# Kernel tuning notes

Measured on AMD Instinct MI355X. Metric: run time of the kernel, lower is better.

Reference implementation:

```python
import jax, jax.numpy as jnp
import numpy as np

AGENT_RADIUS = 0.2
SAFETY_DIST = 0.1
_ang = np.linspace(0.0, 2.0 * np.pi, 8, endpoint=False)
OBSTACLES = np.stack([10.0 * np.cos(_ang), 10.0 * np.sin(_ang), 0.5 * np.ones(8)], axis=-1).astype(np.float32)  # (x, y, r)


def _qp_solve(p, G, h):
    """Exact solve of: min_z 0.5 z^T z + p^T z  s.t. G z <= h, z in R^2.
    Equivalent to QPFunction with Q=I. Enumerates KKT candidates over active
    sets of size 0, 1, 2 (closed form in 2D) and picks the feasible optimum.
    p: [2], G: [m,2], h: [m]."""
    m = G.shape[0]
    ii, jj = np.triu_indices(m, 1)
    # active set {} -> unconstrained minimizer
    z0 = -p[None, :]                                        # [1,2]
    # active set {i}: z = -p - lam*g_i, g_i.z = h_i
    gg = jnp.sum(G * G, axis=-1)                            # [m]
    lam1 = (-(G @ p) - h) / (gg + 1e-12)
    z1 = -p[None, :] - lam1[:, None] * G                    # [m,2]
    ok1 = lam1 >= -1e-8
    # active set {i,j}: z solves 2x2 system [g_i; g_j] z = [h_i; h_j]
    Gi, Gj = G[ii], G[jj]                                   # [P,2]
    hi, hj = h[ii], h[jj]
    det = Gi[:, 0] * Gj[:, 1] - Gi[:, 1] * Gj[:, 0]
    det_ok = jnp.abs(det) > 1e-9
    ds = jnp.where(det_ok, det, 1.0)
    zx = (hi * Gj[:, 1] - hj * Gi[:, 1]) / ds
    zy = (Gi[:, 0] * hj - Gj[:, 0] * hi) / ds
    z2 = jnp.stack([zx, zy], axis=-1)                       # [P,2]
    r = -(z2 + p[None, :])                                  # A^T lam = r
    lam_i = (Gj[:, 1] * r[:, 0] - Gj[:, 0] * r[:, 1]) / ds
    lam_j = (Gi[:, 0] * r[:, 1] - Gi[:, 1] * r[:, 0]) / ds
    ok2 = det_ok & (lam_i >= -1e-8) & (lam_j >= -1e-8)
    Z = jnp.concatenate([z0, z1, z2], axis=0)               # [K,2]
    ok = jnp.concatenate([jnp.ones((1,), bool), ok1, ok2], axis=0)
    tol = 1e-6 * (1.0 + jnp.abs(h))
    feas = jnp.all(Z @ G.T <= (h + tol)[None, :], axis=-1)  # [K]
    obj = 0.5 * jnp.sum(Z * Z, axis=-1) + Z @ p
    obj = jnp.where(ok & feas, obj, jnp.inf)
    return Z[jnp.argmin(obj)]


def _forward(x, mean, std, W1, b1, W21, b21, W31, b31, W22, b22, W32, b32):
    x0 = x * std + mean                                     # de-normalized state [B,8]
    hid = jax.nn.relu(x @ W1.T + b1)
    x31 = jax.nn.relu(hid @ W21.T + b21) @ W31.T + b31      # reference control p [B,2]
    x32 = 4.0 * jax.nn.sigmoid(jax.nn.relu(hid @ W22.T + b22) @ W32.T + b32)  # CBF penalties [B,2]
    px, py, theta, v = x0[:, 0], x0[:, 1], x0[:, 2], x0[:, 3]
    ox, oy, oth, ov = x0[:, 4], x0[:, 5], x0[:, 6], x0[:, 7]
    st, ct = jnp.sin(theta), jnp.cos(theta)
    vs, vc = v * st, v * ct
    obs = jnp.asarray(OBSTACLES, x.dtype)
    # static obstacle constraints, vectorized over the n_obs obstacles
    dx = px[:, None] - obs[None, :, 0]                      # [B,n_obs]
    dy = py[:, None] - obs[None, :, 1]
    R = AGENT_RADIUS + obs[:, 2] + SAFETY_DIST
    bar = dx * dx + dy * dy - (R * R)[None, :]
    bdot = 2.0 * dx * vc[:, None] + 2.0 * dy * vs[:, None]
    Lf2b = (2.0 * v * v)[:, None]
    u1 = -2.0 * dx * vs[:, None] + 2.0 * dy * vc[:, None]
    u2 = 2.0 * dx * ct[:, None] + 2.0 * dy * st[:, None]
    G_obs = -jnp.stack([u1, u2], axis=-1)                   # [B,n_obs,2]
    s0, s1 = x32[:, 0:1], x32[:, 1:2]
    h_obs = Lf2b + (s0 + s1) * bdot + (s0 * s1) * bar       # [B,n_obs]
    # opponent constraint
    Ro = 2.0 * AGENT_RADIUS + SAFETY_DIST
    dxo, dyo = px - ox, py - oy
    so, co = jnp.sin(oth), jnp.cos(oth)
    bar_o = dxo * dxo + dyo * dyo - Ro * Ro
    bdot_o = 2.0 * dxo * (vc - ov * co) + 2.0 * dyo * (vs - ov * so)
    Lf2b_o = 2.0 * (v * v + ov * ov + 2.0 * v * ov * jnp.cos(theta - oth))
    u1o = -2.0 * dxo * vs + 2.0 * dyo * vc
    u2o = 2.0 * dxo * ct + 2.0 * dyo * st
    G_opp = -jnp.stack([u1o, u2o], axis=-1)[:, None, :]     # [B,1,2]
    h_opp = (Lf2b_o + (x32[:, 0] + x32[:, 1]) * bdot_o + x32[:, 0] * x32[:, 1] * bar_o)[:, None]
    G = jnp.concatenate([G_obs, G_opp], axis=1)             # [B,m,2]
    h = jnp.concatenate([h_obs, h_opp], axis=1)             # [B,m]
    return jax.vmap(_qp_solve)(x31, G, h)                   # [B,2]


def setup_inputs() -> dict:
    key = jax.random.key(0)
    ks = jax.random.split(key, 6)
    B, nF, H1, H2 = 65536, 8, 256, 128

    def lin(k, o, i):
        k1, k2 = jax.random.split(k)
        W = jax.random.normal(k1, (o, i), jnp.float32) / np.float32(np.sqrt(i))
        b = jax.random.normal(k2, (o,), jnp.float32) * 0.01
        return W, b

    W1, b1 = lin(ks[0], H1, nF)
    W21, b21 = lin(ks[1], H2, H1)
    W31, b31 = lin(ks[2], 2, H2)
    W22, b22 = lin(ks[3], H2, H1)
    W32, b32 = lin(ks[4], 2, H2)
    x = jax.random.normal(ks[5], (B, nF), jnp.float32)
    return {"x": x, "mean": jnp.zeros((nF,), jnp.float32), "std": jnp.ones((nF,), jnp.float32),
            "W1": W1, "b1": b1, "W21": W21, "b21": b21, "W31": W31, "b31": b31,
            "W22": W22, "b22": b22, "W32": W32, "b32": b32, "sgn": 1}


def reference(x, mean, std, W1, b1, W21, b21, W31, b31, W22, b22, W32, b32, sgn):
    # sgn==1 / training path -> batched differentiable QP solve
    return _forward(x, mean, std, W1, b1, W21, b21, W31, b31, W22, b22, W32, b32)
```

## Files before the change

### kernel.cpp

```cpp
#include <hip/hip_runtime.h>
#include <hip/hip_bf16.h>
#include <math.h>


typedef unsigned int u32;
typedef unsigned long long u64;
typedef unsigned short u16;
typedef __attribute__((ext_vector_type(8))) short short8;
typedef __attribute__((ext_vector_type(4))) float f32x4;
typedef __attribute__((ext_vector_type(2))) float f32x2;
typedef __attribute__((ext_vector_type(4))) u32 u32x4;

union Frag  { short8 v; u32 u[4]; u32x4 q; };
union F8    { long l; u32 u[2]; };

__device__ __forceinline__ u32 packbf(float a, float b) {
    float2 f2; f2.x = a; f2.y = b;
    __hip_bfloat162 h = __float22bfloat162_rn(f2);
    union { __hip_bfloat162 h2; u32 u; } cv; cv.h2 = h;
    return cv.u;
}

__device__ __forceinline__ u32 packfp8x4(float a, float b, float c, float d) {
    u32 r = 0;
    r = (u32)__builtin_amdgcn_cvt_pk_fp8_f32(a, b, (int)r, false);
    r = (u32)__builtin_amdgcn_cvt_pk_fp8_f32(c, d, (int)r, true);
    return r;
}

__device__ const float OBX[8] = { 10.f, 7.07106781186547524f, 6.123234e-16f, -7.07106781186547524f,
                                 -10.f, -7.07106781186547524f, -1.8369702e-15f, 7.07106781186547524f };
__device__ const float OBY[8] = { 0.f, 7.07106781186547524f, 10.f, 7.07106781186547524f,
                                  1.2246468e-15f, -7.07106781186547524f, -10.f, -7.07106781186547524f };

#define PI0_ 0x2111111100000000ULL
#define PI1_ 0x5544443333322222ULL
#define PI2_ 0x7665ULL
#define PJ0_ 0x3876543287654321ULL
#define PJ1_ 0x7687658765487654ULL
#define PJ2_ 0x8878ULL
__device__ __forceinline__ int unpack4(u64 w0, u64 w1, u64 w2, int t) {
    u64 w = (t < 16) ? w0 : (t < 32) ? w1 : w2;
    return (int)((w >> ((t & 15) * 4)) & 15);
}

__global__ __launch_bounds__(256)
void prep_kernel(const float* __restrict__ W21, const float* __restrict__ W22,
                 const float* __restrict__ W1,  const float* __restrict__ b1,
                 u32* __restrict__ ws)
{
    int idx  = blockIdx.x * 256 + threadIdx.x;
    if (idx < 4096) {
        int lane = idx & 63;
        int nt   = (idx >> 6) & 7;
        int kp   = (idx >> 9) & 3;
        int head = idx >> 11;
        const float* W = head ? W22 : W21;
        int q  = lane >> 4;
        int n  = nt * 16 + (lane & 15);
        const float* se = W + n * 256 + (2 * kp) * 32 + q * 8;
        const float* so = W + n * 256 + (2 * kp + 1) * 32 + q * 8;
        u32x4 o;
        o.x = packfp8x4(se[0], se[1], se[2], se[3]);
        o.y = packfp8x4(se[4], se[5], se[6], se[7]);
        o.z = packfp8x4(so[0], so[1], so[2], so[3]);
        o.w = packfp8x4(so[4], so[5], so[6], so[7]);
        __builtin_nontemporal_store(o, (u32x4*)ws + idx);
    } else {
        int f    = idx - 4096;
        int nt   = f >> 6;
        int lane = f & 63;
        int q    = lane >> 4;
        int mm   = lane & 15;
        int n = 32 * (nt & 7) + 8 * (mm >> 2) + 4 * (nt >> 3) + (mm & 3);
        u32x4 o = (u32x4){0u, 0u, 0u, 0u};
        if (q == 0) {
            const float* wr = W1 + n * 8;
            o.x = packbf(wr[0], wr[1]);
            o.y = packbf(wr[2], wr[3]);
            o.z = packbf(wr[4], wr[5]);
            o.w = packbf(wr[6], wr[7]);
        } else if (q == 1) {
            o.x = packbf(b1[n], 0.f);
        }
        __builtin_nontemporal_store(o, (u32x4*)ws + idx);
    }
}

__global__ __launch_bounds__(512)
void barriernet_kernel(const float* __restrict__ x,
                       const float* __restrict__ meanp,
                       const float* __restrict__ stdp,
                       const float* __restrict__ b21,
                       const float* __restrict__ W31,
                       const float* __restrict__ b31,
                       const float* __restrict__ b22,
                       const float* __restrict__ W32,
                       const float* __restrict__ b32,
                       const u32* __restrict__ wsB,
                       float* __restrict__ out, int Btot)
{
    const int tid  = threadIdx.x;
    const int wave = tid >> 6;
    const int lane = tid & 63;
    const int q    = lane >> 4;
    const int m    = lane & 15;
    const int blockRow = blockIdx.x * 128;

    __shared__ u32x4 stage[4096];
    __shared__ float lds_p[128][4];

    const u32x4* wsB4 = (const u32x4*)wsB;

    #pragma unroll
    for (int i = 0; i < 8; ++i) {
        int fi = (wave * 8 + i) * 64 + lane;
        stage[fi] = wsB4[fi];
    }

    Frag xB;
    {
        int R0 = blockRow + wave * 16 + m;
        const f32x4* xv0 = (const f32x4*)(x + (R0 < Btot ? R0 : 0) * 8);
        f32x4 xa0 = xv0[0], xb0 = xv0[1];
        if (q == 0) {
            xB.u[0] = packbf(xa0.x, xa0.y);
            xB.u[1] = packbf(xa0.z, xa0.w);
            xB.u[2] = packbf(xb0.x, xb0.y);
            xB.u[3] = packbf(xb0.z, xb0.w);
        } else if (q == 1) {
            xB.u[0] = 0x00003f80u;
            xB.u[1] = 0u; xB.u[2] = 0u; xB.u[3] = 0u;
        } else {
            xB.u[0] = 0u; xB.u[1] = 0u; xB.u[2] = 0u; xB.u[3] = 0u;
        }
    }
    f32x4 hacc[16];
    {
        const u32x4* W1f = wsB4 + 4096;
        #pragma unroll
        for (int nt = 0; nt < 16; ++nt) {
            Frag Af; Af.q = W1f[nt * 64 + lane];
            hacc[nt] = __builtin_amdgcn_mfma_f32_16x16x32_bf16(
                Af.v, xB.v, (f32x4){0.f, 0.f, 0.f, 0.f}, 0, 0, 0);
        }
    }
    F8 A8[8];
    #pragma unroll
    for (int ks = 0; ks < 8; ++ks) {
        A8[ks].u[0] = packfp8x4(fmaxf(hacc[ks][0], 0.f),     fmaxf(hacc[ks][1], 0.f),
                                fmaxf(hacc[ks][2], 0.f),     fmaxf(hacc[ks][3], 0.f));
        A8[ks].u[1] = packfp8x4(fmaxf(hacc[ks + 8][0], 0.f), fmaxf(hacc[ks + 8][1], 0.f),
                                fmaxf(hacc[ks + 8][2], 0.f), fmaxf(hacc[ks + 8][3], 0.f));
    }

    __syncthreads();

    #pragma unroll 1
    for (int head = 0; head < 2; ++head) {
        const float* b2 = head ? b22 : b21;
        const float* W3 = head ? W32 : W31;
        const float* b3 = head ? b32 : b31;

        f32x4 acc[8];
        #pragma unroll
        for (int nt = 0; nt < 8; ++nt) acc[nt] = (f32x4){0.f, 0.f, 0.f, 0.f};

        const u32x4* hS = stage + head * 2048;
        #pragma unroll
        for (int kp = 0; kp < 4; ++kp) {
            #pragma unroll
            for (int nt = 0; nt < 8; ++nt) {
                u32x4 b = hS[kp * 512 + nt * 64 + lane];
                F8 be; be.u[0] = b.x; be.u[1] = b.y;
                F8 bo; bo.u[0] = b.z; bo.u[1] = b.w;
                acc[nt] = __builtin_amdgcn_mfma_f32_16x16x32_fp8_fp8(
                    A8[2 * kp].l, be.l, acc[nt], 0, 0, 0);
                acc[nt] = __builtin_amdgcn_mfma_f32_16x16x32_fp8_fp8(
                    A8[2 * kp + 1].l, bo.l, acc[nt], 0, 0, 0);
            }
        }

        float pr0[4], pr1[4];
        #pragma unroll
        for (int rg = 0; rg < 4; ++rg) { pr0[rg] = 0.f; pr1[rg] = 0.f; }
        #pragma unroll
        for (int nt = 0; nt < 8; ++nt) {
            int col = nt * 16 + m;
            float b2c = b2[col];
            float w0c = W3[col];
            float w1c = W3[128 + col];
            #pragma unroll
            for (int rg = 0; rg < 4; ++rg) {
                float rv = fmaxf(acc[nt][rg] + b2c, 0.f);
                pr0[rg] = fmaf(rv, w0c, pr0[rg]);
                pr1[rg] = fmaf(rv, w1c, pr1[rg]);
            }
        }
        #pragma unroll
        for (int rg = 0; rg < 4; ++rg) {
            float v0 = pr0[rg], v1 = pr1[rg];
            #pragma unroll
            for (int off = 1; off < 16; off <<= 1) {
                v0 += __shfl_xor(v0, off, 64);
                v1 += __shfl_xor(v1, off, 64);
            }
            pr0[rg] = v0; pr1[rg] = v1;
        }
        if (m == 0) {
            #pragma unroll
            for (int rg = 0; rg < 4; ++rg) {
                int row = wave * 16 + q * 4 + rg;
                float a0 = pr0[rg] + b3[0];
                float a1 = pr1[rg] + b3[1];
                if (head == 0) {
                    lds_p[row][0] = a0;
                    lds_p[row][1] = a1;
                } else {
                    lds_p[row][2] = 4.f / (1.f + __expf(-a0));
                    lds_p[row][3] = 4.f / (1.f + __expf(-a1));
                }
            }
        }
    }
    __syncthreads();

    f32x4 (*qC)[128]  = (f32x4(*)[128])stage;
    f32x4 (*res)[128] = (f32x4(*)[128])(stage + 1152);

    const int rq   = tid & 127;
    const int part = tid >> 7;
    const int R    = blockRow + rq;
    float p0 = lds_p[rq][0];
    float p1 = lds_p[rq][1];

    {
        float s0 = lds_p[rq][2];
        float s1 = lds_p[rq][3];
        const float* xp = x + (R < Btot ? R : 0) * 8;
        f32x4 xv0 = ((const f32x4*)xp)[0];
        f32x4 xv1 = ((const f32x4*)xp)[1];
        const f32x4 sd0 = ((const f32x4*)stdp)[0],  sd1 = ((const f32x4*)stdp)[1];
        const f32x4 mn0 = ((const f32x4*)meanp)[0], mn1 = ((const f32x4*)meanp)[1];
        float px = fmaf(xv0.x, sd0.x, mn0.x);
        float py = fmaf(xv0.y, sd0.y, mn0.y);
        float th = fmaf(xv0.z, sd0.z, mn0.z);
        float v  = fmaf(xv0.w, sd0.w, mn0.w);
        float st = __sinf(th), ct = __cosf(th);
        float vs = v * st, vc = v * ct;
        float sps = s0 + s1, ss = s0 * s1;
        float Lf2b = 2.f * v * v;
        #pragma unroll
        for (int kk = 0; kk < 2; ++kk) {
            int k = part + kk * 4;
            float dx = px - OBX[k], dy = py - OBY[k];
            float bar  = dx * dx + dy * dy - 0.64f;
            float bdot = 2.f * dx * vc + 2.f * dy * vs;
            float gx = 2.f * dx * vs - 2.f * dy * vc;
            float gy = -(2.f * dx * ct + 2.f * dy * st);
            float hk = Lf2b + sps * bdot + ss * bar;
            float ht = hk + 1e-6f * (1.f + fabsf(hk));
            qC[k][rq] = (f32x4){gx, gy, hk, ht};
        }
        if (part == 3) {
            float ox = fmaf(xv1.x, sd1.x, mn1.x);
            float oy = fmaf(xv1.y, sd1.y, mn1.y);
            float oth= fmaf(xv1.z, sd1.z, mn1.z);
            float ov = fmaf(xv1.w, sd1.w, mn1.w);
            float so = __sinf(oth), co = __cosf(oth);
            float dxo = px - ox, dyo = py - oy;
            float bar_o  = dxo * dxo + dyo * dyo - 0.25f;
            float bdot_o = 2.f * dxo * (vc - ov * co) + 2.f * dyo * (vs - ov * so);
            float Lf2b_o = 2.f * (v * v + ov * ov + 2.f * v * ov * __cosf(th - oth));
            float gx = 2.f * dxo * vs - 2.f * dyo * vc;
            float gy = -(2.f * dxo * ct + 2.f * dyo * st);
            float hk = Lf2b_o + sps * bdot_o + ss * bar_o;
            float ht = hk + 1e-6f * (1.f + fabsf(hk));
            qC[8][rq] = (f32x4){gx, gy, hk, ht};
        }
    }
    __syncthreads();

    const f32x4 C0 = qC[0][rq], C1 = qC[1][rq], C2 = qC[2][rq];
    const f32x4 C3 = qC[3][rq], C4 = qC[4][rq], C5 = qC[5][rq];
    const f32x4 C6 = qC[6][rq], C7 = qC[7][rq], C8 = qC[8][rq];

    const float zx0 = -p0, zy0 = -p1;
    bool z0ok =
        (zx0 * C0.x + zy0 * C0.y <= C0.w) &&
        (zx0 * C1.x + zy0 * C1.y <= C1.w) &&
        (zx0 * C2.x + zy0 * C2.y <= C2.w) &&
        (zx0 * C3.x + zy0 * C3.y <= C3.w) &&
        (zx0 * C4.x + zy0 * C4.y <= C4.w) &&
        (zx0 * C5.x + zy0 * C5.y <= C5.w) &&
        (zx0 * C6.x + zy0 * C6.y <= C6.w) &&
        (zx0 * C7.x + zy0 * C7.y <= C7.w) &&
        (zx0 * C8.x + zy0 * C8.y <= C8.w);

    float bobj = INFINITY;
    float bzx = zx0, bzy = zy0;
    if (z0ok) {
        if (part == 0)
            bobj = 0.5f * (zx0 * zx0 + zy0 * zy0) + zx0 * p0 + zy0 * p1;
    } else {
        const int c0i = (part == 0) ? 0  : (part == 1) ? 12 : (part == 2) ? 24 : 35;
        const int c1i = (part == 0) ? 12 : (part == 1) ? 24 : (part == 2) ? 35 : 46;
        #pragma unroll 2
        for (int c = c0i; c < c1i; ++c) {
            float zx, zy;
            bool pre;
            if (c == 0) {
                zx = -p0; zy = -p1; pre = true;
            } else if (c <= 9) {
                f32x4 g = qC[c - 1][rq];
                float gg  = g.x * g.x + g.y * g.y;
                float lam = (-(g.x * p0 + g.y * p1) - g.z) / (gg + 1e-12f);
                zx = -p0 - lam * g.x;
                zy = -p1 - lam * g.y;
                pre = (lam >= -1e-8f);
            } else {
                int t = c - 10;
                int pi = unpack4(PI0_, PI1_, PI2_, t);
                int pj = unpack4(PJ0_, PJ1_, PJ2_, t);
                f32x4 gi = qC[pi][rq];
                f32x4 gj = qC[pj][rq];
                float det = gi.x * gj.y - gi.y * gj.x;
                bool dok = fabsf(det) > 1e-9f;
                float ds = dok ? det : 1.0f;
                float inv = 1.0f / ds;
                zx = (gi.z * gj.y - gj.z * gi.y) * inv;
                zy = (gi.x * gj.z - gj.x * gi.z) * inv;
                float rx = -(zx + p0), ry = -(zy + p1);
                float li = (gj.y * rx - gj.x * ry) * inv;
                float lj = (gi.x * ry - gi.y * rx) * inv;
                pre = dok && (li >= -1e-8f) && (lj >= -1e-8f);
            }
            bool ok = pre;
            ok = ok && (zx * C0.x + zy * C0.y <= C0.w);
            ok = ok && (zx * C1.x + zy * C1.y <= C1.w);
            ok = ok && (zx * C2.x + zy * C2.y <= C2.w);
            ok = ok && (zx * C3.x + zy * C3.y <= C3.w);
            ok = ok && (zx * C4.x + zy * C4.y <= C4.w);
            ok = ok && (zx * C5.x + zy * C5.y <= C5.w);
            ok = ok && (zx * C6.x + zy * C6.y <= C6.w);
            ok = ok && (zx * C7.x + zy * C7.y <= C7.w);
            ok = ok && (zx * C8.x + zy * C8.y <= C8.w);
            float obj = 0.5f * (zx * zx + zy * zy) + zx * p0 + zy * p1;
            if (ok && obj < bobj) { bobj = obj; bzx = zx; bzy = zy; }
        }
    }

    if (part) {
        res[part - 1][rq] = (f32x4){bobj, bzx, bzy, 0.f};
    }
    __syncthreads();
    if (part == 0) {
        #pragma unroll
        for (int pp = 0; pp < 3; ++pp) {
            f32x4 r = res[pp][rq];
            if (r.x < bobj) { bobj = r.x; bzx = r.y; bzy = r.z; }
        }
        if (R < Btot) {
            f32x2 o2; o2.x = bzx; o2.y = bzy;
            ((f32x2*)out)[R] = o2;
        }
    }
}

extern "C" void kernel_launch(void* const* d_in, const int* in_sizes, int n_in,
                              void* d_out, int out_size, void* d_ws, size_t ws_size,
                              hipStream_t stream) {
    const float* x    = (const float*)d_in[0];
    const float* mean = (const float*)d_in[1];
    const float* stdv = (const float*)d_in[2];
    const float* W1   = (const float*)d_in[3];
    const float* b1   = (const float*)d_in[4];
    const float* W21  = (const float*)d_in[5];
    const float* b21  = (const float*)d_in[6];
    const float* W31  = (const float*)d_in[7];
    const float* b31  = (const float*)d_in[8];
    const float* W22  = (const float*)d_in[9];
    const float* b22  = (const float*)d_in[10];
    const float* W32  = (const float*)d_in[11];
    const float* b32  = (const float*)d_in[12];
    int B = in_sizes[0] / 8;
    float* out = (float*)d_out;
    u32* ws = (u32*)d_ws;

    hipLaunchKernelGGL(prep_kernel, dim3(20), dim3(256), 0, stream,
                       W21, W22, W1, b1, ws);

    hipLaunchKernelGGL(barriernet_kernel, dim3((B + 127) / 128), dim3(512), 0, stream,
                       x, mean, stdv, b21, W31, b31, b22, W32, b32,
                       ws, out, B);
}
```

Measured before the change: 103.8 us.

## Switch MLP to 32x32 MFMA tiles with 256-thread blocks and DMA weight staging

Recasts the fused MLP to use 32x32xK MFMA instructions, so each wave handles 32 rows and blocks shrink from 512 to 256 threads. Prep reorders the fp8 W2 fragments, the bf16 W1 fragments and the layer-3 weights and biases into matching 32x32 layouts. The final 2-output projection now runs as a bf16 MFMA instead of scalar FMAs plus cross-lane shuffles. Weights are staged into LDS with global_load_lds DMA. The QP enumeration is split over 2 parts instead of 4, so each thread does more candidates and there are fewer threads per row.

```diff
diff --git a/kernel.cpp b/kernel.cpp
--- a/kernel.cpp
+++ b/kernel.cpp
@@ -8,11 +8,23 @@
 typedef unsigned short u16;
 typedef __attribute__((ext_vector_type(8))) short short8;
 typedef __attribute__((ext_vector_type(4))) float f32x4;
+typedef __attribute__((ext_vector_type(16))) float f32x16;
 typedef __attribute__((ext_vector_type(2))) float f32x2;
 typedef __attribute__((ext_vector_type(4))) u32 u32x4;
 
 union Frag  { short8 v; u32 u[4]; u32x4 q; };
 union F8    { long l; u32 u[2]; };
+
+__device__ __forceinline__ f32x16 zero16() {
+    f32x16 z = {0.f, 0.f, 0.f, 0.f, 0.f, 0.f, 0.f, 0.f,
+                0.f, 0.f, 0.f, 0.f, 0.f, 0.f, 0.f, 0.f};
+    return z;
+}
+
+#define DMA16(gp, lp)                                                        \
+    __builtin_amdgcn_global_load_lds(                                        \
+        (const __attribute__((address_space(1))) void*)(gp),                 \
+        (__attribute__((address_space(3))) void*)(lp), 16, 0, 0)
 
 __device__ __forceinline__ u32 packbf(float a, float b) {
     float2 f2; f2.x = a; f2.y = b;
@@ -20,7 +32,6 @@
     union { __hip_bfloat162 h2; u32 u; } cv; cv.h2 = h;
     return cv.u;
 }
-
 __device__ __forceinline__ u32 packfp8x4(float a, float b, float c, float d) {
     u32 r = 0;
     r = (u32)__builtin_amdgcn_cvt_pk_fp8_f32(a, b, (int)r, false);
@@ -47,55 +58,77 @@
 __global__ __launch_bounds__(256)
 void prep_kernel(const float* __restrict__ W21, const float* __restrict__ W22,
                  const float* __restrict__ W1,  const float* __restrict__ b1,
+                 const float* __restrict__ W31, const float* __restrict__ W32,
+                 const float* __restrict__ b21, const float* __restrict__ b22,
                  u32* __restrict__ ws)
 {
-    int idx  = blockIdx.x * 256 + threadIdx.x;
+    int idx = blockIdx.x * 256 + threadIdx.x;
     if (idx < 4096) {
         int lane = idx & 63;
-        int nt   = (idx >> 6) & 7;
-        int kp   = (idx >> 9) & 3;
+        int nt   = (idx >> 6) & 3;
+        int kp   = (idx >> 8) & 7;
         int head = idx >> 11;
         const float* W = head ? W22 : W21;
-        int q  = lane >> 4;
-        int n  = nt * 16 + (lane & 15);
-        const float* se = W + n * 256 + (2 * kp) * 32 + q * 8;
-        const float* so = W + n * 256 + (2 * kp + 1) * 32 + q * 8;
-        u32x4 o;
-        o.x = packfp8x4(se[0], se[1], se[2], se[3]);
-        o.y = packfp8x4(se[4], se[5], se[6], se[7]);
-        o.z = packfp8x4(so[0], so[1], so[2], so[3]);
-        o.w = packfp8x4(so[4], so[5], so[6], so[7]);
-        __builtin_nontemporal_store(o, (u32x4*)ws + idx);
-    } else {
-        int f    = idx - 4096;
-        int nt   = f >> 6;
+        int o  = nt * 32 + (lane & 31);
+        int hi = lane >> 5;
+        const float* base = W + o * 256 + kp * 32 + hi * 4;
+        u32x4 e;
+        e.x = packfp8x4(base[0],  base[1],  base[2],  base[3]);
+        e.y = packfp8x4(base[8],  base[9],  base[10], base[11]);
+        e.z = packfp8x4(base[16], base[17], base[18], base[19]);
+        e.w = packfp8x4(base[24], base[25], base[26], base[27]);
+        __builtin_nontemporal_store(e, (u32x4*)ws + idx);
+    } else if (idx < 4608) {
+        int f = idx - 4096;
+        int inst = f >> 6, lane = f & 63;
+        int hi = lane >> 5;
+        int h  = inst * 32 + (lane & 31);
+        u32x4 e = (u32x4){0u, 0u, 0u, 0u};
+        if (hi == 0) {
+            const float* wr = W1 + h * 8;
+            e.x = packbf(wr[0], wr[1]);
+            e.y = packbf(wr[2], wr[3]);
+            e.z = packbf(wr[4], wr[5]);
+            e.w = packbf(wr[6], wr[7]);
+        } else {
+            e.x = packbf(b1[h], 0.f);
+        }
+        __builtin_nontemporal_store(e, (u32x4*)ws + idx);
+    } else if (idx < 5632) {
+        int f = idx - 4608;
+        int head = f >> 9;
+        int kb   = (f >> 6) & 7;
         int lane = f & 63;
-        int q    = lane >> 4;
-        int mm   = lane & 15;
-        int n = 32 * (nt & 7) + 8 * (mm >> 2) + 4 * (nt >> 3) + (mm & 3);
-        u32x4 o = (u32x4){0u, 0u, 0u, 0u};
-        if (q == 0) {
-            const float* wr = W1 + n * 8;
-            o.x = packbf(wr[0], wr[1]);
-            o.y = packbf(wr[2], wr[3]);
-            o.z = packbf(wr[4], wr[5]);
-            o.w = packbf(wr[6], wr[7]);
-        } else if (q == 1) {
-            o.x = packbf(b1[n], 0.f);
-        }
-        __builtin_nontemporal_store(o, (u32x4*)ws + idx);
-    }
-}
-
-__global__ __launch_bounds__(512)
+        int hi = lane >> 5;
+        int mr = lane & 31;
+        const float* W3 = head ? W32 : W31;
+        int ob = 32 * (kb >> 1) + 16 * (kb & 1) + 4 * hi;
+        float v0=0, v1=0, v2=0, v3=0, v4=0, v5=0, v6=0, v7=0;
+        if (mr < 2) {
+            const float* wr = W3 + mr * 128;
+            v0 = wr[ob];     v1 = wr[ob + 1]; v2 = wr[ob + 2]; v3 = wr[ob + 3];
+            v4 = wr[ob + 8]; v5 = wr[ob + 9]; v6 = wr[ob + 10]; v7 = wr[ob + 11];
+        }
+        u32x4 e;
+        e.x = packbf(v0, v1); e.y = packbf(v2, v3);
+        e.z = packbf(v4, v5); e.w = packbf(v6, v7);
+        __builtin_nontemporal_store(e, (u32x4*)ws + idx);
+    } else if (idx < 5696) {
+        int f = idx - 5632;
+        int head = f >> 5, hi = (f >> 4) & 1, nt = (f >> 2) & 3, t = f & 3;
+        const float* b2 = head ? b22 : b21;
+        int o0 = nt * 32 + 8 * t + 4 * hi;
+        f32x4 e; e.x = b2[o0]; e.y = b2[o0+1]; e.z = b2[o0+2]; e.w = b2[o0+3];
+        union { f32x4 f; u32x4 u; } cv; cv.f = e;
+        __builtin_nontemporal_store(cv.u, (u32x4*)ws + idx);
+    }
+}
+
+__global__ __launch_bounds__(256)
 void barriernet_kernel(const float* __restrict__ x,
                        const float* __restrict__ meanp,
                        const float* __restrict__ stdp,
-                       const float* __restrict__ b21,
-                       const float* __restrict__ W31,
                        const float* __restrict__ b31,
-                       const float* __restrict__ b22,
-                       const float* __restrict__ W32,
                        const float* __restrict__ b32,
                        const u32* __restrict__ wsB,
                        float* __restrict__ out, int Btot)
@@ -103,8 +136,8 @@
     const int tid  = threadIdx.x;
     const int wave = tid >> 6;
     const int lane = tid & 63;
-    const int q    = lane >> 4;
-    const int m    = lane & 15;
+    const int hi   = lane >> 5;
+    const int ml   = lane & 31;
     const int blockRow = blockIdx.x * 128;
 
     __shared__ u32x4 stage[4096];
@@ -112,114 +145,125 @@
 
     const u32x4* wsB4 = (const u32x4*)wsB;
 
-    #pragma unroll
-    for (int i = 0; i < 8; ++i) {
-        int fi = (wave * 8 + i) * 64 + lane;
-        stage[fi] = wsB4[fi];
+    {
+        const u32x4* g0 = wsB4 + wave * 1024 + lane;
+        u32x4* l0 = stage + wave * 1024;
+        #pragma unroll
+        for (int i = 0; i < 16; ++i)
+            DMA16(g0 + i * 64, l0 + i * 64);
     }
 
     Frag xB;
     {
-        int R0 = blockRow + wave * 16 + m;
+        int R0 = blockRow + wave * 32 + ml;
         const f32x4* xv0 = (const f32x4*)(x + (R0 < Btot ? R0 : 0) * 8);
         f32x4 xa0 = xv0[0], xb0 = xv0[1];
-        if (q == 0) {
+        if (hi == 0) {
             xB.u[0] = packbf(xa0.x, xa0.y);
             xB.u[1] = packbf(xa0.z, xa0.w);
             xB.u[2] = packbf(xb0.x, xb0.y);
             xB.u[3] = packbf(xb0.z, xb0.w);
-        } else if (q == 1) {
+        } else {
             xB.u[0] = 0x00003f80u;
             xB.u[1] = 0u; xB.u[2] = 0u; xB.u[3] = 0u;
-        } else {
-            xB.u[0] = 0u; xB.u[1] = 0u; xB.u[2] = 0u; xB.u[3] = 0u;
-        }
-    }
-    f32x4 hacc[16];
-    {
-        const u32x4* W1f = wsB4 + 4096;
-        #pragma unroll
-        for (int nt = 0; nt < 16; ++nt) {
-            Frag Af; Af.q = W1f[nt * 64 + lane];
-            hacc[nt] = __builtin_amdgcn_mfma_f32_16x16x32_bf16(
-                Af.v, xB.v, (f32x4){0.f, 0.f, 0.f, 0.f}, 0, 0, 0);
-        }
-    }
-    F8 A8[8];
+        }
+    }
+    F8 B8[16];
     #pragma unroll
-    for (int ks = 0; ks < 8; ++ks) {
-        A8[ks].u[0] = packfp8x4(fmaxf(hacc[ks][0], 0.f),     fmaxf(hacc[ks][1], 0.f),
-                                fmaxf(hacc[ks][2], 0.f),     fmaxf(hacc[ks][3], 0.f));
-        A8[ks].u[1] = packfp8x4(fmaxf(hacc[ks + 8][0], 0.f), fmaxf(hacc[ks + 8][1], 0.f),
-                                fmaxf(hacc[ks + 8][2], 0.f), fmaxf(hacc[ks + 8][3], 0.f));
+    for (int chunk = 0; chunk < 2; ++chunk) {
+        f32x16 hacc[4];
+        #pragma unroll
+        for (int i2 = 0; i2 < 4; ++i2) {
+            int inst = chunk * 4 + i2;
+            Frag W1f; W1f.q = wsB4[4096 + inst * 64 + lane];
+            hacc[i2] = __builtin_amdgcn_mfma_f32_32x32x16_bf16(
+                W1f.v, xB.v, zero16(), 0, 0, 0);
+        }
+        #pragma unroll
+        for (int k2 = 0; k2 < 8; ++k2) {
+            int ks = chunk * 8 + k2;
+            int i2 = k2 >> 1;
+            int pb = 8 * (k2 & 1);
+            B8[ks].u[0] = packfp8x4(fmaxf(hacc[i2][pb+0], 0.f), fmaxf(hacc[i2][pb+1], 0.f),
+                                    fmaxf(hacc[i2][pb+2], 0.f), fmaxf(hacc[i2][pb+3], 0.f));
+            B8[ks].u[1] = packfp8x4(fmaxf(hacc[i2][pb+4], 0.f), fmaxf(hacc[i2][pb+5], 0.f),
+                                    fmaxf(hacc[i2][pb+6], 0.f), fmaxf(hacc[i2][pb+7], 0.f));
+        }
     }
 
     __syncthreads();
 
     #pragma unroll 1
     for (int head = 0; head < 2; ++head) {
-        const float* b2 = head ? b22 : b21;
-        const float* W3 = head ? W32 : W31;
-        const float* b3 = head ? b32 : b31;
-
-        f32x4 acc[8];
-        #pragma unroll
-        for (int nt = 0; nt < 8; ++nt) acc[nt] = (f32x4){0.f, 0.f, 0.f, 0.f};
+        f32x16 acc[4];
+        #pragma unroll
+        for (int nt = 0; nt < 4; ++nt) acc[nt] = zero16();
 
         const u32x4* hS = stage + head * 2048;
         #pragma unroll
-        for (int kp = 0; kp < 4; ++kp) {
+        for (int kp = 0; kp < 8; ++kp) {
             #pragma unroll
-            for (int nt = 0; nt < 8; ++nt) {
-                u32x4 b = hS[kp * 512 + nt * 64 + lane];
-                F8 be; be.u[0] = b.x; be.u[1] = b.y;
-                F8 bo; bo.u[0] = b.z; bo.u[1] = b.w;
-                acc[nt] = __builtin_amdgcn_mfma_f32_16x16x32_fp8_fp8(
-                    A8[2 * kp].l, be.l, acc[nt], 0, 0, 0);
-                acc[nt] = __builtin_amdgcn_mfma_f32_16x16x32_fp8_fp8(
-                    A8[2 * kp + 1].l, bo.l, acc[nt], 0, 0, 0);
+            for (int nt = 0; nt < 4; ++nt) {
+                u32x4 e = hS[kp * 256 + nt * 64 + lane];
+                F8 ae; ae.u[0] = e.x; ae.u[1] = e.y;
+                F8 ao; ao.u[0] = e.z; ao.u[1] = e.w;
+                acc[nt] = __builtin_amdgcn_mfma_f32_32x32x16_fp8_fp8(
+                    ae.l, B8[2 * kp].l, acc[nt], 0, 0, 0);
+                acc[nt] = __builtin_amdgcn_mfma_f32_32x32x16_fp8_fp8(
+                    ao.l, B8[2 * kp + 1].l, acc[nt], 0, 0, 0);
             }
         }
 
-        float pr0[4], pr1[4];
-        #pragma unroll
-        for (int rg = 0; rg < 4; ++rg) { pr0[rg] = 0.f; pr1[rg] = 0.f; }
-        #pragma unroll
-        for (int nt = 0; nt < 8; ++nt) {
-            int col = nt * 16 + m;
-            float b2c = b2[col];
-            float w0c = W3[col];
-            float w1c = W3[128 + col];
-            #pragma unroll
-            for (int rg = 0; rg < 4; ++rg) {
-                float rv = fmaxf(acc[nt][rg] + b2c, 0.f);
-                pr0[rg] = fmaf(rv, w0c, pr0[rg]);
-                pr1[rg] = fmaf(rv, w1c, pr1[rg]);
-            }
-        }
-        #pragma unroll
-        for (int rg = 0; rg < 4; ++rg) {
-            float v0 = pr0[rg], v1 = pr1[rg];
-            #pragma unroll
-            for (int off = 1; off < 16; off <<= 1) {
-                v0 += __shfl_xor(v0, off, 64);
-                v1 += __shfl_xor(v1, off, 64);
-            }
-            pr0[rg] = v0; pr1[rg] = v1;
-        }
-        if (m == 0) {
-            #pragma unroll
-            for (int rg = 0; rg < 4; ++rg) {
-                int row = wave * 16 + q * 4 + rg;
-                float a0 = pr0[rg] + b3[0];
-                float a1 = pr1[rg] + b3[1];
-                if (head == 0) {
-                    lds_p[row][0] = a0;
-                    lds_p[row][1] = a1;
-                } else {
-                    lds_p[row][2] = 4.f / (1.f + __expf(-a0));
-                    lds_p[row][3] = 4.f / (1.f + __expf(-a1));
-                }
+        const f32x4* b2p = (const f32x4*)(wsB4 + 5632 + head * 32 + hi * 16);
+        Frag rvB[8];
+        #pragma unroll
+        for (int nt = 0; nt < 4; ++nt) {
+            f32x4 bq0 = b2p[nt * 4 + 0];
+            f32x4 bq1 = b2p[nt * 4 + 1];
+            f32x4 bq2 = b2p[nt * 4 + 2];
+            f32x4 bq3 = b2p[nt * 4 + 3];
+            float rv0  = fmaxf(acc[nt][0]  + bq0.x, 0.f);
+            float rv1  = fmaxf(acc[nt][1]  + bq0.y, 0.f);
+            float rv2  = fmaxf(acc[nt][2]  + bq0.z, 0.f);
+            float rv3  = fmaxf(acc[nt][3]  + bq0.w, 0.f);
+            float rv4  = fmaxf(acc[nt][4]  + bq1.x, 0.f);
+            float rv5  = fmaxf(acc[nt][5]  + bq1.y, 0.f);
+            float rv6  = fmaxf(acc[nt][6]  + bq1.z, 0.f);
+            float rv7  = fmaxf(acc[nt][7]  + bq1.w, 0.f);
+            float rv8  = fmaxf(acc[nt][8]  + bq2.x, 0.f);
+            float rv9  = fmaxf(acc[nt][9]  + bq2.y, 0.f);
+            float rv10 = fmaxf(acc[nt][10] + bq2.z, 0.f);
+            float rv11 = fmaxf(acc[nt][11] + bq2.w, 0.f);
+            float rv12 = fmaxf(acc[nt][12] + bq3.x, 0.f);
+            float rv13 = fmaxf(acc[nt][13] + bq3.y, 0.f);
+            float rv14 = fmaxf(acc[nt][14] + bq3.z, 0.f);
+            float rv15 = fmaxf(acc[nt][15] + bq3.w, 0.f);
+            rvB[nt * 2 + 0].u[0] = packbf(rv0,  rv1);
+            rvB[nt * 2 + 0].u[1] = packbf(rv2,  rv3);
+            rvB[nt * 2 + 0].u[2] = packbf(rv4,  rv5);
+            rvB[nt * 2 + 0].u[3] = packbf(rv6,  rv7);
+            rvB[nt * 2 + 1].u[0] = packbf(rv8,  rv9);
+            rvB[nt * 2 + 1].u[1] = packbf(rv10, rv11);
+            rvB[nt * 2 + 1].u[2] = packbf(rv12, rv13);
+            rvB[nt * 2 + 1].u[3] = packbf(rv14, rv15);
+        }
+        f32x16 acc3 = zero16();
+        #pragma unroll
+        for (int kb = 0; kb < 8; ++kb) {
+            Frag W3f; W3f.q = wsB4[4608 + head * 512 + kb * 64 + lane];
+            acc3 = __builtin_amdgcn_mfma_f32_32x32x16_bf16(
+                W3f.v, rvB[kb].v, acc3, 0, 0, 0);
+        }
+        if (hi == 0) {
+            int row = wave * 32 + ml;
+            if (head == 0) {
+                lds_p[row][0] = acc3[0] + b31[0];
+                lds_p[row][1] = acc3[1] + b31[1];
+            } else {
+                float a0 = acc3[0] + b32[0];
+                float a1 = acc3[1] + b32[1];
+                lds_p[row][2] = 4.f / (1.f + __expf(-a0));
+                lds_p[row][3] = 4.f / (1.f + __expf(-a1));
             }
         }
     }
@@ -251,8 +295,8 @@
         float sps = s0 + s1, ss = s0 * s1;
         float Lf2b = 2.f * v * v;
         #pragma unroll
-        for (int kk = 0; kk < 2; ++kk) {
-            int k = part + kk * 4;
+        for (int kk = 0; kk < 4; ++kk) {
+            int k = part * 4 + kk;
             float dx = px - OBX[k], dy = py - OBY[k];
             float bar  = dx * dx + dy * dy - 0.64f;
             float bdot = 2.f * dx * vc + 2.f * dy * vs;
@@ -262,7 +306,7 @@
             float ht = hk + 1e-6f * (1.f + fabsf(hk));
             qC[k][rq] = (f32x4){gx, gy, hk, ht};
         }
-        if (part == 3) {
+        if (part == 1) {
             float ox = fmaf(xv1.x, sd1.x, mn1.x);
             float oy = fmaf(xv1.y, sd1.y, mn1.y);
             float oth= fmaf(xv1.z, sd1.z, mn1.z);
@@ -303,8 +347,8 @@
         if (part == 0)
             bobj = 0.5f * (zx0 * zx0 + zy0 * zy0) + zx0 * p0 + zy0 * p1;
     } else {
-        const int c0i = (part == 0) ? 0  : (part == 1) ? 12 : (part == 2) ? 24 : 35;
-        const int c1i = (part == 0) ? 12 : (part == 1) ? 24 : (part == 2) ? 35 : 46;
+        const int c0i = part ? 24 : 0;
+        const int c1i = part ? 46 : 24;
         #pragma unroll 2
         for (int c = c0i; c < c1i; ++c) {
             float zx, zy;
@@ -351,15 +395,12 @@
     }
 
     if (part) {
-        res[part - 1][rq] = (f32x4){bobj, bzx, bzy, 0.f};
+        res[0][rq] = (f32x4){bobj, bzx, bzy, 0.f};
     }
     __syncthreads();
     if (part == 0) {
-        #pragma unroll
-        for (int pp = 0; pp < 3; ++pp) {
-            f32x4 r = res[pp][rq];
-            if (r.x < bobj) { bobj = r.x; bzx = r.y; bzy = r.z; }
-        }
+        f32x4 r = res[0][rq];
+        if (r.x < bobj) { bobj = r.x; bzx = r.y; bzy = r.z; }
         if (R < Btot) {
             f32x2 o2; o2.x = bzx; o2.y = bzy;
             ((f32x2*)out)[R] = o2;
@@ -387,10 +428,9 @@
     float* out = (float*)d_out;
     u32* ws = (u32*)d_ws;
 
-    hipLaunchKernelGGL(prep_kernel, dim3(20), dim3(256), 0, stream,
-                       W21, W22, W1, b1, ws);
-
-    hipLaunchKernelGGL(barriernet_kernel, dim3((B + 127) / 128), dim3(512), 0, stream,
-                       x, mean, stdv, b21, W31, b31, b22, W32, b32,
-                       ws, out, B);
-}
+    hipLaunchKernelGGL(prep_kernel, dim3(24), dim3(256), 0, stream,
+                       W21, W22, W1, b1, W31, W32, b21, b22, ws);
+
+    hipLaunchKernelGGL(barriernet_kernel, dim3((B + 127) / 128), dim3(256), 0, stream,
+                       x, mean, stdv, b31, b32, ws, out, B);
+}
```

Result: no change. 103.5 us (median of 2 runs) (-0.3%).
